# Performance work log

Hardware: AMD Instinct MI355X
Metric: run time of the kernel (lower is better)

The kernel has to match this reference:

```python
import jax, jax.numpy as jnp
import numpy as np

EPS = 1e-20
STRIDE, PADDING, DILATION = 1, 2, 1


def setup_inputs() -> dict:
    key = jax.random.key(0)
    ks = jax.random.split(key, 8)
    B, C, O, H, W, K = 8, 32, 32, 256, 256, 5
    return {
        "d": jax.random.uniform(ks[0], (B, C, H, W), jnp.float32) + 0.1,   # positive depth
        "cd": jax.random.uniform(ks[1], (B, C, H, W), jnp.float32),        # depth confidence in [0,1)
        "gx": jax.random.normal(ks[2], (B, C, H, W), jnp.float32),         # x-gradient
        "cgx": jax.random.uniform(ks[3], (B, C, H, W), jnp.float32),       # gradient confidence
        "w_prop": jax.random.normal(ks[4], (1, C, 1, 1), jnp.float32) * 0.1,
        "spatial_weight": jax.random.normal(ks[5], (C, 1, K, K), jnp.float32) * 0.1,
        "channel_weight": jax.random.normal(ks[6], (O, C, 1, 1), jnp.float32) * 0.1,
        "bias": jax.random.normal(ks[7], (1, O, 1, 1), jnp.float32) * 0.01,
    }


def _conv(x, w, groups, stride=1, padding=0, dilation=1):
    return jax.lax.conv_general_dilated(
        x, w, (stride, stride), ((padding, padding), (padding, padding)),
        rhs_dilation=(dilation, dilation),
        dimension_numbers=("NCHW", "OIHW", "NCHW"),
        feature_group_count=groups)


def reference(d, cd, gx, cgx, w_prop, spatial_weight, channel_weight, bias):
    in_channels = d.shape[1]
    # EnforcePos reparameterization: effective weights = softplus(raw)
    wp = jax.nn.softplus(w_prop)
    sw = jax.nn.softplus(spatial_weight)
    cw = jax.nn.softplus(channel_weight)

    pad_w = lambda x, lr: jnp.pad(x, ((0, 0), (0, 0), (0, 0), lr))
    d_left = pad_w(d[..., :-1], (0, 1))
    cd_left = pad_w(cd[..., :-1], (0, 1))
    d_right = pad_w(d[..., 1:], (1, 0))
    cd_right = pad_w(cd[..., 1:], (1, 0))

    cgx_from_ds = cd_left * cd_right
    height = (cd_left * d_left + cd_right * d_right) / (cd_left + cd_right + EPS)
    gx_from_ds = (d_right - d_left) / 2 / (height + EPS)

    gx_prop = (wp * cgx * gx + cgx_from_ds * gx_from_ds) / (wp * cgx + cgx_from_ds + EPS)
    cgx_prop = (wp * cgx + cgx_from_ds) / (wp + 1)

    # depthwise spatial conv (groups = in_channels), then 1x1 channel conv
    nom = _conv(cgx_prop * gx_prop, sw, in_channels, STRIDE, PADDING, DILATION)
    denom = _conv(cgx_prop, sw, in_channels, STRIDE, PADDING, DILATION)
    gx_s = nom / (denom + EPS)
    cgx_s = denom / jnp.sum(sw)

    nom = _conv(cgx_s * gx_s, cw, 1)
    denom = _conv(cgx_s, cw, 1)
    gx_out = nom / (denom + EPS) + bias
    cgx_out = denom / jnp.sum(cw)
    return (gx_out * STRIDE, cgx_out / (STRIDE * STRIDE))
```

## Files before the change

kernel.cpp:

```cpp
#include <hip/hip_runtime.h>
#include <math.h>

constexpr int IMG_H = 256;
constexpr int IMG_W = 256;
constexpr int NB = 8;
constexpr int NC = 32;
constexpr int NO = 32;
constexpr int PLANE = IMG_H * IMG_W;
constexpr int HALF = NB * NC * PLANE;

constexpr int TW = 16;
constexpr int TH = 32;
constexpr int NT = TW * TH;
constexpr int RR = TH + 4;
constexpr int RCF = 24;
constexpr int RSB = RCF * 4;
constexpr int PXB = RR * RSB;
constexpr int BUFB = 2 * PXB;
constexpr int NTASK = RR * 12;
constexpr int TILES = (IMG_W / TW) * (IMG_H / TH);

#define EPSV 1e-20f

typedef float f4 __attribute__((ext_vector_type(4)));
typedef float f2 __attribute__((ext_vector_type(2)));

__device__ __forceinline__ float rcpf_(float x) { return __builtin_amdgcn_rcpf(x); }
__device__ __forceinline__ float softplusf_(float x) {
  return fmaxf(x, 0.0f) + log1pf(expf(-fabsf(x)));
}

__global__ void weights_kernel(const float* __restrict__ wp_raw,
                               const float* __restrict__ sw_raw,
                               const float* __restrict__ cw_raw,
                               float* __restrict__ ws) {
  __shared__ float red[256];
  const int t = threadIdx.x;
  if (t < 32) ws[t] = softplusf_(wp_raw[t]);
  float ssum = 0.f;
  for (int i = t; i < NC * 25; i += 256) {
    float v = softplusf_(sw_raw[i]);
    ws[32 + i] = v;
    ssum += v;
  }
  float csum = 0.f;
  for (int i = t; i < NO * NC; i += 256) {
    float v = softplusf_(cw_raw[i]);
    int o = i >> 5, c = i & 31;
    ws[832 + c * NO + o] = v;
    csum += v;
  }
  red[t] = ssum; __syncthreads();
  for (int off = 128; off; off >>= 1) { if (t < off) red[t] += red[t + off]; __syncthreads(); }
  const float S_sw = red[0];
  __syncthreads();
  red[t] = csum; __syncthreads();
  for (int off = 128; off; off >>= 1) { if (t < off) red[t] += red[t + off]; __syncthreads(); }
  if (t == 0) { ws[1856] = S_sw; ws[1857] = red[0]; }
}

__device__ __forceinline__ void pointwise_pv(
    float dv, float cdv, float gxv, float cgv, int gw,
    float wpc, float inv_wp1, float& Pv, float& Vv) {
  float dl  = (gw == IMG_W - 1) ? 0.f : dv;
  float cdl = (gw == IMG_W - 1) ? 0.f : cdv;
  float dr  = (gw == 0) ? 0.f : dv;
  float cdr = (gw == 0) ? 0.f : cdv;
  float cfd = cdl * cdr;
  float height = (cdl * dl + cdr * dr) * rcpf_(cdl + cdr + EPSV);
  float gfd = (dr - dl) * 0.5f * rcpf_(height + EPSV);
  float den = fmaf(wpc, cgv, cfd);
  float num = fmaf(wpc * cgv, gxv, cfd * gfd);
  float gprop = num * rcpf_(den + EPSV);
  float cprop = den * inv_wp1;
  Pv = cprop;
  Vv = cprop * gprop;
}

__global__ __launch_bounds__(NT, 4) void fused_kernel(
    const float* __restrict__ dp, const float* __restrict__ cdp,
    const float* __restrict__ gxp, const float* __restrict__ cgxp,
    const float* __restrict__ ws, const float* __restrict__ bias,
    float* __restrict__ out) {
  __shared__ __align__(16) char shb[2 * BUFB];

  const int t = threadIdx.x;

  const int wg = blockIdx.x + blockIdx.y * gridDim.x;
  const int virt = (wg & 7) * TILES + (wg >> 3);
  const int b = virt >> 7;
  const int tile = virt & (TILES - 1);
  const int tx = tile & 15, ty = tile >> 4;
  const int w0 = tx * TW, h0 = ty * TH;

  const float Ssw = ws[1856], Scw = ws[1857];
  const float epsS = EPSV * Ssw;
  const float oscale = rcpf_(Ssw) * rcpf_(Scw);

  const bool tact = t < NTASK;
  const int R = min(t, NTASK - 1) / 12;
  const int hq = min(t, NTASK - 1) - R * 12;
  const int gh = h0 + R - 2;
  const int ghc = min(max(gh, 0), IMG_H - 1);
  const int g0 = w0 - 4 + 2 * hq;
  const int g0c = min(max(g0, 0), IMG_W - 2);
  const int goff = ghc * IMG_W + g0c;
  const bool rowv = (unsigned)gh < (unsigned)IMG_H;
  const float m0 = (rowv & ((unsigned)g0 < (unsigned)IMG_W)) ? 1.f : 0.f;
  const float m1 = (rowv & ((unsigned)(g0 + 1) < (unsigned)IMG_W)) ? 1.f : 0.f;
  const int wb = R * RSB + hq * 8;

  const int x = t & (TW - 1);
  const int r = t >> 4;
  const int cvb = r * RSB + (x + 2) * 4;
  const int pixoff = (h0 + r) * IMG_W + (w0 + x);

  const int planebase = b * NC * PLANE;

  float accN[32], accD[32];
  #pragma unroll
  for (int o = 0; o < 32; ++o) { accN[o] = 0.f; accD[o] = 0.f; }

  f2 vd, vc, vg, vx;
  if (tact) {
    vd = *(const f2*)(dp + planebase + goff);
    vc = *(const f2*)(cdp + planebase + goff);
    vg = *(const f2*)(gxp + planebase + goff);
    vx = *(const f2*)(cgxp + planebase + goff);
  }

  #pragma unroll 1
  for (int c = 0; c < NC; ++c) {
    const int bsel = (c & 1) * BUFB;
    const float wpc = ws[c];
    const float inv_wp1 = rcpf_(wpc + 1.0f);

    if (tact) {
      float P0, V0, P1, V1;
      pointwise_pv(vd[0], vc[0] * m0, vg[0], vx[0] * m0, g0,
                   wpc, inv_wp1, P0, V0);
      pointwise_pv(vd[1], vc[1] * m1, vg[1], vx[1] * m1, g0 + 1,
                   wpc, inv_wp1, P1, V1);
      f2 Pw; Pw[0] = P0; Pw[1] = P1;
      f2 Vw; Vw[0] = V0; Vw[1] = V1;
      *(f2*)(shb + bsel + wb) = Pw;
      *(f2*)(shb + bsel + PXB + wb) = Vw;
    }

    if ((c + 1 < NC) & tact) {
      const int pb = planebase + (c + 1) * PLANE + goff;
      vd = *(const f2*)(dp + pb);
      vc = *(const f2*)(cdp + pb);
      vg = *(const f2*)(gxp + pb);
      vx = *(const f2*)(cgxp + pb);
    }

    __syncthreads();

    const char* bp = shb + bsel + cvb;
    const float* swc = ws + 32 + c * 25;
    float Dc = 0.f, Nc = 0.f;
    #pragma unroll
    for (int kr = 0; kr < 5; ++kr) {
      #pragma unroll
      for (int kc = 0; kc < 5; ++kc) {
        const float wv = swc[kr * 5 + kc];
        const float pv = *(const float*)(bp + kr * RSB + kc * 4);
        const float vv = *(const float*)(bp + PXB + kr * RSB + kc * 4);
        Dc = fmaf(wv, pv, Dc);
        Nc = fmaf(wv, vv, Nc);
      }
    }

    const float* cwc = ws + 832 + c * NO;
    #pragma unroll
    for (int o = 0; o < 32; ++o) {
      const float wv = cwc[o];
      accD[o] = fmaf(wv, Dc, accD[o]);
      accN[o] = fmaf(wv, Nc, accN[o]);
    }
  }

  const int ob = b * NO * PLANE + pixoff;
  #pragma unroll
  for (int o = 0; o < 32; ++o) {
    const float g = fmaf(accN[o], rcpf_(accD[o] + epsS), bias[o]);
    const float cg = accD[o] * oscale;
    out[ob + o * PLANE] = g;
    out[HALF + ob + o * PLANE] = cg;
  }
}

extern "C" void kernel_launch(void* const* d_in, const int* in_sizes, int n_in,
                              void* d_out, int out_size, void* d_ws, size_t ws_size,
                              hipStream_t stream) {
  const float* dp   = (const float*)d_in[0];
  const float* cdp  = (const float*)d_in[1];
  const float* gxp  = (const float*)d_in[2];
  const float* cgxp = (const float*)d_in[3];
  const float* wp   = (const float*)d_in[4];
  const float* sw   = (const float*)d_in[5];
  const float* cw   = (const float*)d_in[6];
  const float* bias = (const float*)d_in[7];
  float* out = (float*)d_out;
  float* ws  = (float*)d_ws;

  weights_kernel<<<1, 256, 0, stream>>>(wp, sw, cw, ws);
  fused_kernel<<<dim3(TILES, NB), NT, 0, stream>>>(dp, cdp, gxp, cgxp, ws,
                                                   bias, out);
}
```

Baseline: 390.0 us.

## Process two channels per barrier with wider 32x8 tiles and redistributed staging

Changes the tile from 16x32 to 32x8 so each block has 256 threads and a smaller halo row stride. The channel loop now handles two channels per iteration, with staging tasks spread across all threads for two channel planes. This halves the number of __syncthreads and double-buffers pairs of channels in four shared buffers. The cost is more halo overhead per output pixel (12 halo rows over 8 output rows), more shared memory, and more register pressure from holding two prefetched channel sets.

```diff
diff --git a/kernel.cpp b/kernel.cpp
--- a/kernel.cpp
+++ b/kernel.cpp
@@ -9,16 +9,17 @@
 constexpr int PLANE = IMG_H * IMG_W;
 constexpr int HALF = NB * NC * PLANE;
 
-constexpr int TW = 16;
-constexpr int TH = 32;
+constexpr int TW = 32;
+constexpr int TH = 8;
 constexpr int NT = TW * TH;
 constexpr int RR = TH + 4;
-constexpr int RCF = 24;
-constexpr int RSB = RCF * 4;
+constexpr int RC = 40;
+constexpr int RSB = RC * 4;
 constexpr int PXB = RR * RSB;
 constexpr int BUFB = 2 * PXB;
-constexpr int NTASK = RR * 12;
+constexpr int NTASK = RR * 20;
 constexpr int TILES = (IMG_W / TW) * (IMG_H / TH);
+constexpr int NBLK = TILES * NB;
 
 #define EPSV 1e-20f
 
@@ -77,41 +78,71 @@
   Vv = cprop * gprop;
 }
 
+struct TaskGeo {
+  int goff;
+  int gc0;
+  float m0, m1;
+  int wb;
+};
+
+__device__ __forceinline__ TaskGeo make_geo(int task, int h0, int w0) {
+  TaskGeo G;
+  const int R = task / 20;
+  const int hq = task - R * 20;
+  const int gh = h0 + R - 2;
+  const int ghc = min(max(gh, 0), IMG_H - 1);
+  const int g0 = w0 - 4 + 2 * hq;
+  const int g0c = min(max(g0, 0), IMG_W - 2);
+  G.goff = ghc * IMG_W + g0c;
+  G.gc0 = g0;
+  const bool rowv = (unsigned)gh < (unsigned)IMG_H;
+  G.m0 = (rowv & ((unsigned)g0 < (unsigned)IMG_W)) ? 1.f : 0.f;
+  G.m1 = (rowv & ((unsigned)(g0 + 1) < (unsigned)IMG_W)) ? 1.f : 0.f;
+  G.wb = R * RSB + hq * 8;
+  return G;
+}
+
+__device__ __forceinline__ void stage_pv(f2 vd, f2 vc, f2 vg, f2 vx,
+                                         const TaskGeo& G, float wpc,
+                                         float inv_wp1, char* dst) {
+  float P0, V0, P1, V1;
+  pointwise_pv(vd[0], vc[0] * G.m0, vg[0], vx[0] * G.m0, G.gc0,
+               wpc, inv_wp1, P0, V0);
+  pointwise_pv(vd[1], vc[1] * G.m1, vg[1], vx[1] * G.m1, G.gc0 + 1,
+               wpc, inv_wp1, P1, V1);
+  f2 Pw; Pw[0] = P0; Pw[1] = P1;
+  f2 Vw; Vw[0] = V0; Vw[1] = V1;
+  *(f2*)(dst + G.wb) = Pw;
+  *(f2*)(dst + PXB + G.wb) = Vw;
+}
+
 __global__ __launch_bounds__(NT, 4) void fused_kernel(
     const float* __restrict__ dp, const float* __restrict__ cdp,
     const float* __restrict__ gxp, const float* __restrict__ cgxp,
     const float* __restrict__ ws, const float* __restrict__ bias,
     float* __restrict__ out) {
-  __shared__ __align__(16) char shb[2 * BUFB];
+  __shared__ __align__(16) char shb[4 * BUFB];
 
   const int t = threadIdx.x;
 
-  const int wg = blockIdx.x + blockIdx.y * gridDim.x;
+  const int wg = blockIdx.x;
   const int virt = (wg & 7) * TILES + (wg >> 3);
-  const int b = virt >> 7;
+  const int b = virt >> 8;
   const int tile = virt & (TILES - 1);
-  const int tx = tile & 15, ty = tile >> 4;
+  const int tx = tile & 7, ty = tile >> 3;
   const int w0 = tx * TW, h0 = ty * TH;
 
   const float Ssw = ws[1856], Scw = ws[1857];
   const float epsS = EPSV * Ssw;
   const float oscale = rcpf_(Ssw) * rcpf_(Scw);
 
-  const bool tact = t < NTASK;
-  const int R = min(t, NTASK - 1) / 12;
-  const int hq = min(t, NTASK - 1) - R * 12;
-  const int gh = h0 + R - 2;
-  const int ghc = min(max(gh, 0), IMG_H - 1);
-  const int g0 = w0 - 4 + 2 * hq;
-  const int g0c = min(max(g0, 0), IMG_W - 2);
-  const int goff = ghc * IMG_W + g0c;
-  const bool rowv = (unsigned)gh < (unsigned)IMG_H;
-  const float m0 = (rowv & ((unsigned)g0 < (unsigned)IMG_W)) ? 1.f : 0.f;
-  const float m1 = (rowv & ((unsigned)(g0 + 1) < (unsigned)IMG_W)) ? 1.f : 0.f;
-  const int wb = R * RSB + hq * 8;
+  const int f0 = (t >= NTASK) ? 1 : 0;
+  const TaskGeo G0 = make_geo(t - NTASK * f0, h0, w0);
+  const bool act1 = (t < 2 * NTASK - NT);
+  const TaskGeo G1 = make_geo(min(t + (NT - NTASK), NTASK - 1), h0, w0);
 
   const int x = t & (TW - 1);
-  const int r = t >> 4;
+  const int r = t >> 5;
   const int cvb = r * RSB + (x + 2) * 4;
   const int pixoff = (h0 + r) * IMG_W + (w0 + x);
 
@@ -121,63 +152,70 @@
   #pragma unroll
   for (int o = 0; o < 32; ++o) { accN[o] = 0.f; accD[o] = 0.f; }
 
-  f2 vd, vc, vg, vx;
-  if (tact) {
-    vd = *(const f2*)(dp + planebase + goff);
-    vc = *(const f2*)(cdp + planebase + goff);
-    vg = *(const f2*)(gxp + planebase + goff);
-    vx = *(const f2*)(cgxp + planebase + goff);
+  f2 d0, c0, g0v, x0, d1, c1, g1v, x1;
+  {
+    const int p0 = planebase + (0 + f0) * PLANE + G0.goff;
+    d0 = *(const f2*)(dp + p0);  c0 = *(const f2*)(cdp + p0);
+    g0v = *(const f2*)(gxp + p0); x0 = *(const f2*)(cgxp + p0);
+    if (act1) {
+      const int p1 = planebase + 1 * PLANE + G1.goff;
+      d1 = *(const f2*)(dp + p1);  c1 = *(const f2*)(cdp + p1);
+      g1v = *(const f2*)(gxp + p1); x1 = *(const f2*)(cgxp + p1);
+    }
   }
 
   #pragma unroll 1
-  for (int c = 0; c < NC; ++c) {
-    const int bsel = (c & 1) * BUFB;
-    const float wpc = ws[c];
-    const float inv_wp1 = rcpf_(wpc + 1.0f);
-
-    if (tact) {
-      float P0, V0, P1, V1;
-      pointwise_pv(vd[0], vc[0] * m0, vg[0], vx[0] * m0, g0,
-                   wpc, inv_wp1, P0, V0);
-      pointwise_pv(vd[1], vc[1] * m1, vg[1], vx[1] * m1, g0 + 1,
-                   wpc, inv_wp1, P1, V1);
-      f2 Pw; Pw[0] = P0; Pw[1] = P1;
-      f2 Vw; Vw[0] = V0; Vw[1] = V1;
-      *(f2*)(shb + bsel + wb) = Pw;
-      *(f2*)(shb + bsel + PXB + wb) = Vw;
-    }
-
-    if ((c + 1 < NC) & tact) {
-      const int pb = planebase + (c + 1) * PLANE + goff;
-      vd = *(const f2*)(dp + pb);
-      vc = *(const f2*)(cdp + pb);
-      vg = *(const f2*)(gxp + pb);
-      vx = *(const f2*)(cgxp + pb);
+  for (int g = 0; g < NC; g += 2) {
+    const int q = (g >> 1) & 1;
+    char* bufA = shb + (2 * q) * BUFB;
+    char* bufB = shb + (2 * q + 1) * BUFB;
+
+    const float wpA = ws[g], wpB = ws[g + 1];
+    const float invA = rcpf_(wpA + 1.0f), invB = rcpf_(wpB + 1.0f);
+    const float wp0 = f0 ? wpB : wpA;
+    const float inv0 = f0 ? invB : invA;
+
+    stage_pv(d0, c0, g0v, x0, G0, wp0, inv0, f0 ? bufB : bufA);
+    if (act1) stage_pv(d1, c1, g1v, x1, G1, wpB, invB, bufB);
+
+    if (g + 2 < NC) {
+      const int p0 = planebase + (g + 2 + f0) * PLANE + G0.goff;
+      d0 = *(const f2*)(dp + p0);  c0 = *(const f2*)(cdp + p0);
+      g0v = *(const f2*)(gxp + p0); x0 = *(const f2*)(cgxp + p0);
+      if (act1) {
+        const int p1 = planebase + (g + 3) * PLANE + G1.goff;
+        d1 = *(const f2*)(dp + p1);  c1 = *(const f2*)(cdp + p1);
+        g1v = *(const f2*)(gxp + p1); x1 = *(const f2*)(cgxp + p1);
+      }
     }
 
     __syncthreads();
 
-    const char* bp = shb + bsel + cvb;
-    const float* swc = ws + 32 + c * 25;
-    float Dc = 0.f, Nc = 0.f;
+    const char* bpA = bufA + cvb;
+    const char* bpB = bufB + cvb;
+    const float* swA = ws + 32 + g * 25;
+    const float* swB = swA + 25;
+    float DA = 0.f, NA = 0.f, DB = 0.f, NBv = 0.f;
     #pragma unroll
     for (int kr = 0; kr < 5; ++kr) {
       #pragma unroll
       for (int kc = 0; kc < 5; ++kc) {
-        const float wv = swc[kr * 5 + kc];
-        const float pv = *(const float*)(bp + kr * RSB + kc * 4);
-        const float vv = *(const float*)(bp + PXB + kr * RSB + kc * 4);
-        Dc = fmaf(wv, pv, Dc);
-        Nc = fmaf(wv, vv, Nc);
+        const int off = kr * RSB + kc * 4;
+        const float wA = swA[kr * 5 + kc];
+        const float wB = swB[kr * 5 + kc];
+        DA  = fmaf(wA, *(const float*)(bpA + off), DA);
+        NA  = fmaf(wA, *(const float*)(bpA + PXB + off), NA);
+        DB  = fmaf(wB, *(const float*)(bpB + off), DB);
+        NBv = fmaf(wB, *(const float*)(bpB + PXB + off), NBv);
       }
     }
 
-    const float* cwc = ws + 832 + c * NO;
+    const float* cwA = ws + 832 + g * NO;
+    const float* cwB = cwA + NO;
     #pragma unroll
     for (int o = 0; o < 32; ++o) {
-      const float wv = cwc[o];
-      accD[o] = fmaf(wv, Dc, accD[o]);
-      accN[o] = fmaf(wv, Nc, accN[o]);
+      accD[o] = fmaf(cwB[o], DB, fmaf(cwA[o], DA, accD[o]));
+      accN[o] = fmaf(cwB[o], NBv, fmaf(cwA[o], NA, accN[o]));
     }
   }
 
@@ -206,6 +244,5 @@
   float* ws  = (float*)d_ws;
 
   weights_kernel<<<1, 256, 0, stream>>>(wp, sw, cw, ws);
-  fused_kernel<<<dim3(TILES, NB), NT, 0, stream>>>(dp, cdp, gxp, cgxp, ws,
-                                                   bias, out);
-}
+  fused_kernel<<<NBLK, NT, 0, stream>>>(dp, cdp, gxp, cgxp, ws, bias, out);
+}
```

Measured after the change: 404.3 us. +3.7%, slower.

## Give each wave a private 16x4 tile to drop block barriers

Applied to the files above, without the earlier changes.

The kernel is restructured so each 64-lane wave owns a private 16x4 output tile with its own double-buffered LDS region. The block-wide __syncthreads is replaced by a wave-local lgkmcnt wait. P and V are interleaved in LDS so the stencil reads one f2 per tap, and the staging loads use f4 global loads. The cost is a larger halo: each wave loads and recomputes 8x24 inputs for 64 outputs, which adds redundant pointwise work and more L2 traffic.

```diff
diff --git a/kernel.cpp b/kernel.cpp
--- a/kernel.cpp
+++ b/kernel.cpp
@@ -9,16 +9,16 @@
 constexpr int PLANE = IMG_H * IMG_W;
 constexpr int HALF = NB * NC * PLANE;
 
-constexpr int TW = 16;
-constexpr int TH = 32;
-constexpr int NT = TW * TH;
-constexpr int RR = TH + 4;
-constexpr int RCF = 24;
-constexpr int RSB = RCF * 4;
-constexpr int PXB = RR * RSB;
-constexpr int BUFB = 2 * PXB;
-constexpr int NTASK = RR * 12;
-constexpr int TILES = (IMG_W / TW) * (IMG_H / TH);
+constexpr int WTW = 16;
+constexpr int WTH = 4;
+constexpr int RR = WTH + 4;
+constexpr int RC = 24;
+constexpr int RSB = RC * 8;
+constexpr int BUFB = RR * RSB;
+constexpr int WLDS = 2 * BUFB;
+constexpr int NWAVE = 4;
+constexpr int NT = NWAVE * 64;
+constexpr int NBLK = (IMG_W / WTW) * (IMG_H / WTH) * NB / NWAVE;
 
 #define EPSV 1e-20f
 
@@ -82,102 +82,105 @@
     const float* __restrict__ gxp, const float* __restrict__ cgxp,
     const float* __restrict__ ws, const float* __restrict__ bias,
     float* __restrict__ out) {
-  __shared__ __align__(16) char shb[2 * BUFB];
+  __shared__ __align__(16) char shb[NWAVE * WLDS];
 
   const int t = threadIdx.x;
-
-  const int wg = blockIdx.x + blockIdx.y * gridDim.x;
-  const int virt = (wg & 7) * TILES + (wg >> 3);
-  const int b = virt >> 7;
-  const int tile = virt & (TILES - 1);
-  const int tx = tile & 15, ty = tile >> 4;
-  const int w0 = tx * TW, h0 = ty * TH;
+  const int wid = t >> 6;
+  const int lane = t & 63;
+  char* wbase = shb + wid * WLDS;
+
+  const int wg = blockIdx.x;
+  const int virt = (wg & 7) * (NBLK / 8) + (wg >> 3);
+  const int b = virt >> 8;
+  const int rem = virt & 255;
+  const int ty = rem >> 2;
+  const int qx = rem & 3;
+  const int tx = qx * 4 + wid;
+  const int w0 = tx * WTW, h0 = ty * WTH;
 
   const float Ssw = ws[1856], Scw = ws[1857];
   const float epsS = EPSV * Ssw;
   const float oscale = rcpf_(Ssw) * rcpf_(Scw);
 
-  const bool tact = t < NTASK;
-  const int R = min(t, NTASK - 1) / 12;
-  const int hq = min(t, NTASK - 1) - R * 12;
-  const int gh = h0 + R - 2;
+  const bool sact = lane < 48;
+  const int Rr = min(lane, 47) / 6;
+  const int qq = min(lane, 47) - 6 * Rr;
+  const int gh = h0 + Rr - 2;
   const int ghc = min(max(gh, 0), IMG_H - 1);
-  const int g0 = w0 - 4 + 2 * hq;
-  const int g0c = min(max(g0, 0), IMG_W - 2);
-  const int goff = ghc * IMG_W + g0c;
+  const int gc0 = w0 - 4 + 4 * qq;
+  const int gc0c = min(max(gc0, 0), IMG_W - 4);
+  const int goff = ghc * IMG_W + gc0c;
   const bool rowv = (unsigned)gh < (unsigned)IMG_H;
-  const float m0 = (rowv & ((unsigned)g0 < (unsigned)IMG_W)) ? 1.f : 0.f;
-  const float m1 = (rowv & ((unsigned)(g0 + 1) < (unsigned)IMG_W)) ? 1.f : 0.f;
-  const int wb = R * RSB + hq * 8;
-
-  const int x = t & (TW - 1);
-  const int r = t >> 4;
-  const int cvb = r * RSB + (x + 2) * 4;
-  const int pixoff = (h0 + r) * IMG_W + (w0 + x);
-
+  float msk[4];
+  #pragma unroll
+  for (int j = 0; j < 4; ++j)
+    msk[j] = (rowv & ((unsigned)(gc0 + j) < (unsigned)IMG_W)) ? 1.f : 0.f;
+  const int wb = Rr * RSB + qq * 32;
+
+  const int x = lane & 15, y = lane >> 4;
+  const int cvb = y * RSB + (x + 2) * 8;
+  const int pixoff = (h0 + y) * IMG_W + (w0 + x);
   const int planebase = b * NC * PLANE;
 
   float accN[32], accD[32];
   #pragma unroll
   for (int o = 0; o < 32; ++o) { accN[o] = 0.f; accD[o] = 0.f; }
 
-  f2 vd, vc, vg, vx;
-  if (tact) {
-    vd = *(const f2*)(dp + planebase + goff);
-    vc = *(const f2*)(cdp + planebase + goff);
-    vg = *(const f2*)(gxp + planebase + goff);
-    vx = *(const f2*)(cgxp + planebase + goff);
+  f4 rd, rc, rg, rx;
+  if (sact) {
+    rd = *(const f4*)(dp + planebase + goff);
+    rc = *(const f4*)(cdp + planebase + goff);
+    rg = *(const f4*)(gxp + planebase + goff);
+    rx = *(const f4*)(cgxp + planebase + goff);
   }
 
   #pragma unroll 1
   for (int c = 0; c < NC; ++c) {
-    const int bsel = (c & 1) * BUFB;
+    char* buf = wbase + (c & 1) * BUFB;
     const float wpc = ws[c];
     const float inv_wp1 = rcpf_(wpc + 1.0f);
 
-    if (tact) {
-      float P0, V0, P1, V1;
-      pointwise_pv(vd[0], vc[0] * m0, vg[0], vx[0] * m0, g0,
-                   wpc, inv_wp1, P0, V0);
-      pointwise_pv(vd[1], vc[1] * m1, vg[1], vx[1] * m1, g0 + 1,
-                   wpc, inv_wp1, P1, V1);
-      f2 Pw; Pw[0] = P0; Pw[1] = P1;
-      f2 Vw; Vw[0] = V0; Vw[1] = V1;
-      *(f2*)(shb + bsel + wb) = Pw;
-      *(f2*)(shb + bsel + PXB + wb) = Vw;
-    }
-
-    if ((c + 1 < NC) & tact) {
+    if (sact) {
+      float P[4], V[4];
+      #pragma unroll
+      for (int j = 0; j < 4; ++j)
+        pointwise_pv(rd[j], rc[j] * msk[j], rg[j], rx[j] * msk[j], gc0 + j,
+                     wpc, inv_wp1, P[j], V[j]);
+      f4 wv1; wv1[0] = P[0]; wv1[1] = V[0]; wv1[2] = P[1]; wv1[3] = V[1];
+      f4 wv2; wv2[0] = P[2]; wv2[1] = V[2]; wv2[2] = P[3]; wv2[3] = V[3];
+      *(f4*)(buf + wb) = wv1;
+      *(f4*)(buf + wb + 16) = wv2;
+    }
+
+    if ((c + 1 < NC) & sact) {
       const int pb = planebase + (c + 1) * PLANE + goff;
-      vd = *(const f2*)(dp + pb);
-      vc = *(const f2*)(cdp + pb);
-      vg = *(const f2*)(gxp + pb);
-      vx = *(const f2*)(cgxp + pb);
-    }
-
-    __syncthreads();
-
-    const char* bp = shb + bsel + cvb;
+      rd = *(const f4*)(dp + pb);
+      rc = *(const f4*)(cdp + pb);
+      rg = *(const f4*)(gxp + pb);
+      rx = *(const f4*)(cgxp + pb);
+    }
+
+    asm volatile("s_waitcnt lgkmcnt(0)" ::: "memory");
+
+    const char* bp = buf + cvb;
     const float* swc = ws + 32 + c * 25;
     float Dc = 0.f, Nc = 0.f;
     #pragma unroll
     for (int kr = 0; kr < 5; ++kr) {
       #pragma unroll
       for (int kc = 0; kc < 5; ++kc) {
+        const f2 pv = *(const f2*)(bp + kr * RSB + kc * 8);
         const float wv = swc[kr * 5 + kc];
-        const float pv = *(const float*)(bp + kr * RSB + kc * 4);
-        const float vv = *(const float*)(bp + PXB + kr * RSB + kc * 4);
-        Dc = fmaf(wv, pv, Dc);
-        Nc = fmaf(wv, vv, Nc);
+        Dc = fmaf(wv, pv[0], Dc);
+        Nc = fmaf(wv, pv[1], Nc);
       }
     }
 
     const float* cwc = ws + 832 + c * NO;
     #pragma unroll
     for (int o = 0; o < 32; ++o) {
-      const float wv = cwc[o];
-      accD[o] = fmaf(wv, Dc, accD[o]);
-      accN[o] = fmaf(wv, Nc, accN[o]);
+      accD[o] = fmaf(cwc[o], Dc, accD[o]);
+      accN[o] = fmaf(cwc[o], Nc, accN[o]);
     }
   }
 
@@ -206,6 +209,5 @@
   float* ws  = (float*)d_ws;
 
   weights_kernel<<<1, 256, 0, stream>>>(wp, sw, cw, ws);
-  fused_kernel<<<dim3(TILES, NB), NT, 0, stream>>>(dp, cdp, gxp, cgxp, ws,
-                                                   bias, out);
-}
+  fused_kernel<<<NBLK, NT, 0, stream>>>(dp, cdp, gxp, cgxp, ws, bias, out);
+}
```

New measurement: 405.7 us. 4.0% more time.

## Interleave P/V in LDS and use packed float2 math for conv accumulation

Applied to the files above, without the earlier changes.

Stores the P and V planes interleaved as float2 pairs in shared memory, so each 5x5 tap needs one 64-bit LDS read and the accumulations can use packed FMA. The cprop*gprop product is simplified algebraically to num*inv_wp1, which drops a reciprocal per pixel. The next-channel global prefetch moves after the barrier, launch bounds drop from 4 to 3, and the grid is flattened to 1D. Packed math may cut VALU and LDS instruction counts, while the lower occupancy target gives more registers but fewer waves to hide latency.

```diff
diff --git a/kernel.cpp b/kernel.cpp
--- a/kernel.cpp
+++ b/kernel.cpp
@@ -13,10 +13,9 @@
 constexpr int TH = 32;
 constexpr int NT = TW * TH;
 constexpr int RR = TH + 4;
-constexpr int RCF = 24;
-constexpr int RSB = RCF * 4;
-constexpr int PXB = RR * RSB;
-constexpr int BUFB = 2 * PXB;
+constexpr int RC = 24;
+constexpr int RSB = RC * 8;
+constexpr int BUFB = RR * RSB;
 constexpr int NTASK = RR * 12;
 constexpr int TILES = (IMG_W / TW) * (IMG_H / TH);
 
@@ -71,13 +70,11 @@
   float gfd = (dr - dl) * 0.5f * rcpf_(height + EPSV);
   float den = fmaf(wpc, cgv, cfd);
   float num = fmaf(wpc * cgv, gxv, cfd * gfd);
-  float gprop = num * rcpf_(den + EPSV);
-  float cprop = den * inv_wp1;
-  Pv = cprop;
-  Vv = cprop * gprop;
-}
-
-__global__ __launch_bounds__(NT, 4) void fused_kernel(
+  Pv = den * inv_wp1;
+  Vv = num * inv_wp1;
+}
+
+__global__ __launch_bounds__(NT, 3) void fused_kernel(
     const float* __restrict__ dp, const float* __restrict__ cdp,
     const float* __restrict__ gxp, const float* __restrict__ cgxp,
     const float* __restrict__ ws, const float* __restrict__ bias,
@@ -86,7 +83,7 @@
 
   const int t = threadIdx.x;
 
-  const int wg = blockIdx.x + blockIdx.y * gridDim.x;
+  const int wg = blockIdx.x;
   const int virt = (wg & 7) * TILES + (wg >> 3);
   const int b = virt >> 7;
   const int tile = virt & (TILES - 1);
@@ -97,9 +94,10 @@
   const float epsS = EPSV * Ssw;
   const float oscale = rcpf_(Ssw) * rcpf_(Scw);
 
-  const bool tact = t < NTASK;
-  const int R = min(t, NTASK - 1) / 12;
-  const int hq = min(t, NTASK - 1) - R * 12;
+  const bool sact = t < NTASK;
+  const int task = min(t, NTASK - 1);
+  const int R = task / 12;
+  const int hq = task - R * 12;
   const int gh = h0 + R - 2;
   const int ghc = min(max(gh, 0), IMG_H - 1);
   const int g0 = w0 - 4 + 2 * hq;
@@ -108,21 +106,20 @@
   const bool rowv = (unsigned)gh < (unsigned)IMG_H;
   const float m0 = (rowv & ((unsigned)g0 < (unsigned)IMG_W)) ? 1.f : 0.f;
   const float m1 = (rowv & ((unsigned)(g0 + 1) < (unsigned)IMG_W)) ? 1.f : 0.f;
-  const int wb = R * RSB + hq * 8;
+  const int wb = R * RSB + hq * 16;
 
   const int x = t & (TW - 1);
   const int r = t >> 4;
-  const int cvb = r * RSB + (x + 2) * 4;
+  const int cvb = r * RSB + (x + 2) * 8;
   const int pixoff = (h0 + r) * IMG_W + (w0 + x);
-
   const int planebase = b * NC * PLANE;
 
-  float accN[32], accD[32];
+  f2 accDN[32];
   #pragma unroll
-  for (int o = 0; o < 32; ++o) { accN[o] = 0.f; accD[o] = 0.f; }
+  for (int o = 0; o < 32; ++o) accDN[o] = f2{0.f, 0.f};
 
   f2 vd, vc, vg, vx;
-  if (tact) {
+  if (sact) {
     vd = *(const f2*)(dp + planebase + goff);
     vc = *(const f2*)(cdp + planebase + goff);
     vg = *(const f2*)(gxp + planebase + goff);
@@ -131,23 +128,23 @@
 
   #pragma unroll 1
   for (int c = 0; c < NC; ++c) {
-    const int bsel = (c & 1) * BUFB;
+    char* buf = shb + (c & 1) * BUFB;
     const float wpc = ws[c];
     const float inv_wp1 = rcpf_(wpc + 1.0f);
 
-    if (tact) {
+    if (sact) {
       float P0, V0, P1, V1;
       pointwise_pv(vd[0], vc[0] * m0, vg[0], vx[0] * m0, g0,
                    wpc, inv_wp1, P0, V0);
       pointwise_pv(vd[1], vc[1] * m1, vg[1], vx[1] * m1, g0 + 1,
                    wpc, inv_wp1, P1, V1);
-      f2 Pw; Pw[0] = P0; Pw[1] = P1;
-      f2 Vw; Vw[0] = V0; Vw[1] = V1;
-      *(f2*)(shb + bsel + wb) = Pw;
-      *(f2*)(shb + bsel + PXB + wb) = Vw;
+      f4 w; w[0] = P0; w[1] = V0; w[2] = P1; w[3] = V1;
+      *(f4*)(buf + wb) = w;
     }
 
-    if ((c + 1 < NC) & tact) {
+    __syncthreads();
+
+    if ((c + 1 < NC) & sact) {
       const int pb = planebase + (c + 1) * PLANE + goff;
       vd = *(const f2*)(dp + pb);
       vc = *(const f2*)(cdp + pb);
@@ -155,39 +152,31 @@
       vx = *(const f2*)(cgxp + pb);
     }
 
-    __syncthreads();
-
-    const char* bp = shb + bsel + cvb;
+    const char* bp = buf + cvb;
     const float* swc = ws + 32 + c * 25;
-    float Dc = 0.f, Nc = 0.f;
+    f2 dn = f2{0.f, 0.f};
     #pragma unroll
     for (int kr = 0; kr < 5; ++kr) {
       #pragma unroll
       for (int kc = 0; kc < 5; ++kc) {
-        const float wv = swc[kr * 5 + kc];
-        const float pv = *(const float*)(bp + kr * RSB + kc * 4);
-        const float vv = *(const float*)(bp + PXB + kr * RSB + kc * 4);
-        Dc = fmaf(wv, pv, Dc);
-        Nc = fmaf(wv, vv, Nc);
+        const f2 pv = *(const f2*)(bp + kr * RSB + kc * 8);
+        dn += pv * swc[kr * 5 + kc];
       }
     }
 
     const float* cwc = ws + 832 + c * NO;
     #pragma unroll
-    for (int o = 0; o < 32; ++o) {
-      const float wv = cwc[o];
-      accD[o] = fmaf(wv, Dc, accD[o]);
-      accN[o] = fmaf(wv, Nc, accN[o]);
-    }
+    for (int o = 0; o < 32; ++o)
+      accDN[o] += dn * cwc[o];
+
   }
 
   const int ob = b * NO * PLANE + pixoff;
   #pragma unroll
   for (int o = 0; o < 32; ++o) {
-    const float g = fmaf(accN[o], rcpf_(accD[o] + epsS), bias[o]);
-    const float cg = accD[o] * oscale;
-    out[ob + o * PLANE] = g;
-    out[HALF + ob + o * PLANE] = cg;
+    const float D = accDN[o][0], N = accDN[o][1];
+    out[ob + o * PLANE] = fmaf(N, rcpf_(D + epsS), bias[o]);
+    out[HALF + ob + o * PLANE] = D * oscale;
   }
 }
 
@@ -206,6 +195,6 @@
   float* ws  = (float*)d_ws;
 
   weights_kernel<<<1, 256, 0, stream>>>(wp, sw, cw, ws);
-  fused_kernel<<<dim3(TILES, NB), NT, 0, stream>>>(dp, cdp, gxp, cgxp, ws,
-                                                   bias, out);
-}
+  fused_kernel<<<TILES * NB, NT, 0, stream>>>(dp, cdp, gxp, cgxp, ws, bias,
+                                              out);
+}
```

New measurement: 396.7 us. No clear change (+1.7%).
